# Kernel tuning notes

Hardware: AMD Instinct MI355X
Metric: run time of the kernel (lower is better)

Reference implementation:

```python
import jax, jax.numpy as jnp
import numpy as np

K = 16  # number of neighbors (excluding self)


def setup_inputs() -> dict:
    key = jax.random.key(0)
    k0, k1, k2, k3, k4 = jax.random.split(key, 5)
    B, C, N, Cout = 8, 64, 4096, 64
    x = jax.random.normal(k0, (B, C, N), dtype=jnp.float32)
    s = 1.0 / np.sqrt(C).astype(np.float32)
    W1 = jax.random.normal(k1, (Cout, C), dtype=jnp.float32) * s
    b1 = jax.random.normal(k2, (Cout,), dtype=jnp.float32) * 0.01
    W2 = jax.random.normal(k3, (Cout, C), dtype=jnp.float32) * s
    b2 = jax.random.normal(k4, (Cout,), dtype=jnp.float32) * 0.01
    return {"x": x, "W1": W1, "b1": b1, "W2": W2, "b2": b2}


def _knn_idx(xt):
    # xt: [B, N, C]; squared-euclidean self-KNN, drop self (first / smallest dist)
    sq = jnp.sum(xt * xt, axis=-1)                              # [B, N]
    dist = sq[:, :, None] + sq[:, None, :] - 2.0 * jnp.einsum('bnc,bmc->bnm', xt, xt)
    _, idx = jax.lax.top_k(-dist, K + 1)                        # [B, N, K+1]
    return idx[:, :, 1:]                                        # [B, N, K]


def reference(x, W1, b1, W2, b2):
    # x: [B, C, N]
    xt = jnp.transpose(x, (0, 2, 1))                            # [B, N, C]
    idx = _knn_idx(xt)                                          # [B, N, K]
    # gather neighbors: nb[b,n,k,c] = xt[b, idx[b,n,k], c]
    nb = jax.vmap(lambda xb, ib: xb[ib])(xt, idx)               # [B, N, K, C]
    diff = nb - xt[:, :, None, :]                               # [B, N, K, C]
    message = jnp.einsum('bnkc,oc->bnko', diff, W1) + b1        # conv1 (1x1)
    x_center = jnp.einsum('bnc,oc->bno', xt, W2) + b2           # conv2 (1x1)
    edge = jax.nn.relu(x_center[:, :, None, :] + message)       # [B, N, K, Cout]
    y = jnp.max(edge, axis=2)                                   # [B, N, Cout]
    return jnp.transpose(y, (0, 2, 1))[:, :, None, :]           # [B, Cout, 1, N]
```

## Files before the change

### kernel.cpp

```cpp
#include <hip/hip_runtime.h>
#include <hip/hip_bf16.h>
#include <cstdint>

#define NB    8
#define NPTS  4096
#define NQ    4
#define NT    64
#define PROW  64
#define SENT  0xFF000000u
#define KNN_T 512

typedef __attribute__((ext_vector_type(8))) short bf16x8;
typedef __attribute__((ext_vector_type(4))) float f32x4;

__global__ __launch_bounds__(256) void k_prep(const float* __restrict__ x,
                                              const float* __restrict__ W1,
                                              const float* __restrict__ b1,
                                              const float* __restrict__ W2,
                                              const float* __restrict__ b2,
                                              float* __restrict__ xt,
                                              __hip_bfloat16* __restrict__ xh,
                                              __hip_bfloat16* __restrict__ xl,
                                              float* __restrict__ sq,
                                              float* __restrict__ sqn,
                                              __hip_bfloat16* __restrict__ gh,
                                              __hip_bfloat16* __restrict__ gl,
                                              float* __restrict__ bb) {
  const int t = threadIdx.x;
  if (blockIdx.x == 64) {
    if (blockIdx.y != 0) return;
#pragma unroll 1
    for (int i = t; i < 128 * 64; i += 256) {
      int o = i >> 6, c = i & 63;
      float g = (o < 64) ? W1[o * 64 + c]
                         : (W2[(o - 64) * 64 + c] - W1[(o - 64) * 64 + c]);
      __hip_bfloat16 h = __float2bfloat16(g);
      gh[i] = h;
      gl[i] = __float2bfloat16(g - __bfloat162float(h));
    }
    if (t < 64) bb[t] = b1[t] + b2[t];
    return;
  }
  __shared__ float tile[64][65];
  const int b  = blockIdx.y;
  const int n0 = blockIdx.x * 64;
#pragma unroll
  for (int i = 0; i < 16; ++i) {
    int lin = i * 256 + t;
    int c = lin >> 6, j = lin & 63;
    tile[j][c] = x[(size_t)b * 64 * NPTS + (size_t)c * NPTS + n0 + j];
  }
  __syncthreads();
#pragma unroll
  for (int i = 0; i < 16; ++i) {
    int lin = i * 256 + t;
    int j = lin >> 6, c = lin & 63;
    float v = tile[j][c];
    size_t o = ((size_t)b * NPTS + n0 + j) * 64 + c;
    xt[o] = v;
    __hip_bfloat16 h = __float2bfloat16(v);
    xh[o] = h;
    xl[o] = __float2bfloat16(v - __bfloat162float(h));
  }
  if (t < 64) {
    float s = 0.f;
#pragma unroll
    for (int c = 0; c < 64; ++c) { float v = tile[t][c]; s = fmaf(v, v, s); }
    sq [b * NPTS + t + n0] = s;
    sqn[b * NPTS + t + n0] = 0.5f * s;
  }
}

struct Frag { bf16x8 h0, h1; f32x4 sv; };

__global__ __launch_bounds__(KNN_T, 4) void k_knn(const __hip_bfloat16* __restrict__ xh,
                                                  const float* __restrict__ sqn,
                                                  unsigned* __restrict__ part) {
  __shared__ unsigned bufu[17 * KNN_T];

  const int tid  = threadIdx.x;
  const int w    = tid >> 6;
  const int lane = tid & 63;
  const int quad = lane >> 4, l15 = lane & 15;
  const int rb   = blockIdx.x;
  const int q    = blockIdx.y;
  const int b    = blockIdx.z;
  const size_t xbase = (size_t)b * NPTS * 64;
  const int c0   = q * 1024;
  const int nrow = rb * (KNN_T / 4) + w * 16 + l15;

  const __hip_bfloat16* ph = xh + xbase + (size_t)nrow * 64 + quad * 8;
  bf16x8 rh0 = *(const bf16x8*)(ph);
  bf16x8 rh1 = *(const bf16x8*)(ph + 32);
  rh0 = rh0 ^ (short)0x8000;
  rh1 = rh1 ^ (short)0x8000;
  const float srh = sqn[b * NPTS + nrow];

  unsigned D[16];
#pragma unroll
  for (int i = 0; i < 16; ++i) D[i] = SENT;
  unsigned thr = SENT | 0xFFFu;
  int cnt = 0;

  auto ldfrag = [&](int t) -> Frag {
    Frag f;
    const __hip_bfloat16* ah = xh + xbase + (size_t)(c0 + t * 16 + l15) * 64 + quad * 8;
    f.h0 = *(const bf16x8*)(ah);
    f.h1 = *(const bf16x8*)(ah + 32);
    f.sv = *(const f32x4*)(sqn + b * NPTS + c0 + t * 16 + quad * 4);
    return f;
  };

  auto flush = [&]() {
    unsigned E[16];
#pragma unroll
    for (int j = 0; j < 16; ++j) E[j] = bufu[j * KNN_T + tid];
#pragma unroll
    for (int j = 0; j < 16; ++j) E[j] = (j < cnt) ? E[j] : 0xFFFFFFFFu;
#pragma unroll
    for (int k = 2; k <= 16; k <<= 1)
#pragma unroll
      for (int j = k >> 1; j > 0; j >>= 1)
#pragma unroll
        for (int i = 0; i < 16; ++i) {
          int l = i ^ j;
          if (l > i) {
            unsigned lo = min(E[i], E[l]), hi = max(E[i], E[l]);
            bool up = ((i & k) == 0);
            E[i] = up ? lo : hi;
            E[l] = up ? hi : lo;
          }
        }
    unsigned T[16];
#pragma unroll
    for (int i = 0; i < 16; ++i) T[i] = min(D[i], E[15 - i]);
#pragma unroll
    for (int j = 8; j > 0; j >>= 1)
#pragma unroll
      for (int i = 0; i < 16; ++i) {
        int l = i ^ j;
        if (l > i) {
          unsigned lo = min(T[i], T[l]);
          T[l] = max(T[i], T[l]);
          T[i] = lo;
        }
      }
#pragma unroll
    for (int i = 0; i < 16; ++i) D[i] = T[i];
    cnt = 0;
    thr = D[15] | 0xFFFu;
  };

  auto ins = [&](float s, int m) {
    unsigned u = __float_as_uint(s);
    bool pass = (u <= thr);
    int slot = pass ? cnt : 16;
    bufu[slot * KNN_T + tid] = (u & 0xFFFFF000u) | (unsigned)m;
    cnt += pass;
  };

  auto compute2 = [&](const Frag& fa, const Frag& fb, int tbase) {
    f32x4 m1 = fa.sv, m3 = fb.sv;
#pragma unroll
    for (int i = 0; i < 4; ++i) { m1[i] += srh; m3[i] += srh; }
    m1 = __builtin_amdgcn_mfma_f32_16x16x32_bf16(fa.h0, rh0, m1, 0, 0, 0);
    m3 = __builtin_amdgcn_mfma_f32_16x16x32_bf16(fb.h0, rh0, m3, 0, 0, 0);
    m1 = __builtin_amdgcn_mfma_f32_16x16x32_bf16(fa.h1, rh1, m1, 0, 0, 0);
    m3 = __builtin_amdgcn_mfma_f32_16x16x32_bf16(fb.h1, rh1, m3, 0, 0, 0);
    const int cb = c0 + tbase * 16 + quad * 4;
#pragma unroll
    for (int i = 0; i < 4; ++i) ins(m1[i], cb + i);
#pragma unroll
    for (int i = 0; i < 4; ++i) ins(m3[i], cb + 16 + i);
  };

  Frag a0 = ldfrag(0), a1 = ldfrag(1);
#pragma unroll 1
  for (int it = 0; it < 16; ++it) {
    const int t4 = it * 4;
    Frag b0 = ldfrag(t4 + 2), b1 = ldfrag(t4 + 3);
    compute2(a0, a1, t4);
    if (__any(cnt >= 9)) flush();
    const int tn = (t4 + 4 < NT) ? t4 + 4 : 62;
    a0 = ldfrag(tn);
    a1 = ldfrag(tn + 1);
    compute2(b0, b1, t4 + 2);
    if (__any(cnt >= 9)) flush();
  }
  flush();

#pragma unroll
  for (int rd = 0; rd < 2; ++rd) {
    const int dx = (rd == 0) ? 16 : 32;
    unsigned Bx[16], T[16];
#pragma unroll
    for (int i = 0; i < 16; ++i) Bx[i] = (unsigned)__shfl_xor((int)D[i], dx);
#pragma unroll
    for (int i = 0; i < 16; ++i) T[i] = min(D[i], Bx[15 - i]);
#pragma unroll
    for (int j = 8; j > 0; j >>= 1)
#pragma unroll
      for (int i = 0; i < 16; ++i) {
        int l = i ^ j;
        if (l > i) {
          unsigned lo = min(T[i], T[l]);
          T[l] = max(T[i], T[l]);
          T[i] = lo;
        }
      }
#pragma unroll
    for (int i = 0; i < 16; ++i) D[i] = T[i];
  }
  if (quad == 0) {
    const size_t base = (size_t)(b * NPTS + nrow) * PROW + (size_t)q * 16;
#pragma unroll
    for (int i = 0; i < 16; ++i) part[base + i] = D[i];
  }
}

__global__ __launch_bounds__(256) void k_mr(const unsigned* __restrict__ part,
                                            const float* __restrict__ xt,
                                            const float* __restrict__ sq,
                                            int* __restrict__ knn) {
  __shared__ unsigned short lc[8][20];
  const int g   = threadIdx.x >> 5;
  const int c   = threadIdx.x & 31;
  const int row = blockIdx.x * 8 + g;
  const unsigned v0 = part[(size_t)row * PROW + c];
  const unsigned v1 = part[(size_t)row * PROW + 32 + c];
  int r0 = 0, r1 = 0;
#pragma unroll
  for (int j = 0; j < 32; ++j) {
    unsigned a = (unsigned)__shfl((int)v0, j, 32);
    unsigned d = (unsigned)__shfl((int)v1, j, 32);
    r0 += (a < v0) + (d < v0);
    r1 += (a < v1) + (d < v1);
  }
  if (r0 < 20) lc[g][r0] = (unsigned short)(v0 & 0xFFFu);
  if (r1 < 20) lc[g][r1] = (unsigned short)(v1 & 0xFFFu);
  __syncthreads();
  const int b = row >> 12;
  const int m = lc[g][c < 20 ? c : 0];
  const float4* cr = (const float4*)(xt + (size_t)row * 64);
  const float4* mr = (const float4*)(xt + ((size_t)(b << 12) + m) * 64);
  float d = 0.f;
#pragma unroll
  for (int j = 0; j < 16; ++j) {
    float4 a = cr[j], v = mr[j];
    d = fmaf(a.x, v.x, d); d = fmaf(a.y, v.y, d);
    d = fmaf(a.z, v.z, d); d = fmaf(a.w, v.w, d);
  }
  float key = sq[(b << 12) + m] - 2.f * d;
  if (m == (row & 4095)) key = 1e30f;
  int rk = 0;
#pragma unroll
  for (int j = 0; j < 20; ++j) {
    float kj = __shfl(key, j, 32);
    int   mj = __shfl(m, j, 32);
    rk += (kj < key) || ((kj == key) && (mj < m));
  }
  if (c < 20 && rk < 16) knn[(size_t)row * 16 + rk] = m;
}

__global__ __launch_bounds__(256) void k_pq(const __hip_bfloat16* __restrict__ xh,
                                            const __hip_bfloat16* __restrict__ xl,
                                            const __hip_bfloat16* __restrict__ gh,
                                            const __hip_bfloat16* __restrict__ gl,
                                            const float* __restrict__ bb,
                                            float* __restrict__ P,
                                            float* __restrict__ Q) {
  const int tid  = threadIdx.x;
  const int w    = tid >> 6;
  const int lane = tid & 63;
  const int quad = lane >> 4, l15 = lane & 15;
  const int row0 = blockIdx.x * 64 + w * 16;

  const __hip_bfloat16* pa = xh + (size_t)(row0 + l15) * 64 + quad * 8;
  const __hip_bfloat16* pb = xl + (size_t)(row0 + l15) * 64 + quad * 8;
  const bf16x8 ah0 = *(const bf16x8*)(pa);
  const bf16x8 ah1 = *(const bf16x8*)(pa + 32);
  const bf16x8 al0 = *(const bf16x8*)(pb);
  const bf16x8 al1 = *(const bf16x8*)(pb + 32);

#pragma unroll
  for (int ct = 0; ct < 8; ++ct) {
    const __hip_bfloat16* qh = gh + (size_t)(ct * 16 + l15) * 64 + quad * 8;
    const __hip_bfloat16* ql = gl + (size_t)(ct * 16 + l15) * 64 + quad * 8;
    bf16x8 bh0 = *(const bf16x8*)(qh);
    bf16x8 bh1 = *(const bf16x8*)(qh + 32);
    bf16x8 bl0 = *(const bf16x8*)(ql);
    bf16x8 bl1 = *(const bf16x8*)(ql + 32);
    f32x4 m1 = { 0.f, 0.f, 0.f, 0.f };
    f32x4 m2 = m1, m3 = m1, m4 = m1, m5 = m1, m6 = m1;
    m1 = __builtin_amdgcn_mfma_f32_16x16x32_bf16(ah0, bh0, m1, 0, 0, 0);
    m2 = __builtin_amdgcn_mfma_f32_16x16x32_bf16(ah1, bh1, m2, 0, 0, 0);
    m3 = __builtin_amdgcn_mfma_f32_16x16x32_bf16(ah0, bl0, m3, 0, 0, 0);
    m4 = __builtin_amdgcn_mfma_f32_16x16x32_bf16(ah1, bl1, m4, 0, 0, 0);
    m5 = __builtin_amdgcn_mfma_f32_16x16x32_bf16(al0, bh0, m5, 0, 0, 0);
    m6 = __builtin_amdgcn_mfma_f32_16x16x32_bf16(al1, bh1, m6, 0, 0, 0);
    if (ct < 4) {
#pragma unroll
      for (int i = 0; i < 4; ++i) {
        float s = ((m1[i] + m2[i]) + (m3[i] + m4[i])) + (m5[i] + m6[i]);
        P[(size_t)(row0 + quad * 4 + i) * 64 + ct * 16 + l15] = s;
      }
    } else {
      const float bq = bb[(ct - 4) * 16 + l15];
#pragma unroll
      for (int i = 0; i < 4; ++i) {
        float s = ((m1[i] + m2[i]) + (m3[i] + m4[i])) + (m5[i] + m6[i]);
        Q[(size_t)(row0 + quad * 4 + i) * 64 + (ct - 4) * 16 + l15] = s + bq;
      }
    }
  }
}

__global__ __launch_bounds__(512) void k_out(const float* __restrict__ P,
                                             const float* __restrict__ Q,
                                             const int* __restrict__ knn,
                                             float* __restrict__ out) {
  __shared__ float tile[64][65];
  const int b    = blockIdx.y;
  const int n0   = blockIdx.x * 64;
  const int wave = threadIdx.x >> 6;
  const int lane = threadIdx.x & 63;
#pragma unroll 1
  for (int i = 0; i < 8; ++i) {
    const int nl = wave * 8 + i;
    const int gn = b * NPTS + n0 + nl;
    float acc = -1e30f;
    const float qv = Q[(size_t)gn * 64 + lane];
    const int* id = knn + (size_t)gn * 16;
#pragma unroll
    for (int k = 0; k < 16; ++k) {
      int m = id[k];
      float p = P[((size_t)b * NPTS + m) * 64 + lane];
      acc = fmaxf(acc, qv + p);
    }
    tile[nl][lane] = fmaxf(acc, 0.f);
  }
  __syncthreads();
#pragma unroll
  for (int i = 0; i < 8; ++i) {
    const int o = i * 8 + wave;
    out[((size_t)b * 64 + o) * NPTS + n0 + lane] = tile[lane][o];
  }
}

extern "C" void kernel_launch(void* const* d_in, const int* in_sizes, int n_in,
                              void* d_out, int out_size, void* d_ws, size_t ws_size,
                              hipStream_t stream) {
  const float* x  = (const float*)d_in[0];
  const float* W1 = (const float*)d_in[1];
  const float* b1 = (const float*)d_in[2];
  const float* W2 = (const float*)d_in[3];
  const float* b2 = (const float*)d_in[4];
  float* out = (float*)d_out;

  float* ws = (float*)d_ws;
  const size_t NPT_ALL = (size_t)NB * NPTS;
  float*          XT   = ws;
  float*          SQ   = XT + NPT_ALL * 64;
  float*          SQN  = SQ + NPT_ALL;
  __hip_bfloat16* XH   = (__hip_bfloat16*)(SQN + NPT_ALL);
  __hip_bfloat16* XL   = XH + NPT_ALL * 64;
  unsigned*       PART = (unsigned*)(XL + NPT_ALL * 64);
  int*            KNN  = (int*)(PART + NPT_ALL * PROW);
  __hip_bfloat16* GH   = (__hip_bfloat16*)(KNN + NPT_ALL * 16);
  __hip_bfloat16* GL   = GH + 128 * 64;
  float*          BB   = (float*)(GL + 128 * 64);
  float*          Pm   = (float*)PART;
  float*          Qm   = XT;

  k_prep <<<dim3(NPTS / 64 + 1, NB), 256, 0, stream>>>(x, W1, b1, W2, b2,
                                                       XT, XH, XL, SQ, SQN,
                                                       GH, GL, BB);
  k_knn  <<<dim3(NPTS / (KNN_T / 4), NQ, NB), KNN_T, 0, stream>>>(XH, SQN, PART);
  k_mr   <<<dim3(NPT_ALL / 8), 256, 0, stream>>>(PART, XT, SQ, KNN);
  k_pq   <<<dim3(NPT_ALL / 64), 256, 0, stream>>>(XH, XL, GH, GL, BB, Pm, Qm);
  k_out  <<<dim3(NPTS / 64, NB), 512, 0, stream>>>(Pm, Qm, KNN, out);
}
```

Measured before the change: 296.0 us.

## Encode KNN distance as scaled integer key and stagger wave column order

The KNN score is rescaled so that 128*sq + 32768 minus 256*dot (via a bf16 exponent bump on the negated row fragment) becomes a non-negative float. It is truncated to an integer and packed with the column index into a sortable key. This drops the per-element srh add and the float-bit masking, but quantizes distances to integer steps and assumes the value stays within 20 bits. Each wave also starts its column-tile sweep at a different offset, which spreads L2/cache access across waves. The merge kernel now reads its partial rows with a vectorized uint2 load.

```diff
diff --git a/kernel.cpp b/kernel.cpp
--- a/kernel.cpp
+++ b/kernel.cpp
@@ -67,7 +67,7 @@
 #pragma unroll
     for (int c = 0; c < 64; ++c) { float v = tile[t][c]; s = fmaf(v, v, s); }
     sq [b * NPTS + t + n0] = s;
-    sqn[b * NPTS + t + n0] = 0.5f * s;
+    sqn[b * NPTS + t + n0] = fmaf(128.f, s, 32768.f);
   }
 }
 
@@ -87,14 +87,14 @@
   const int b    = blockIdx.z;
   const size_t xbase = (size_t)b * NPTS * 64;
   const int c0   = q * 1024;
+  const int woff = w * 8;
   const int nrow = rb * (KNN_T / 4) + w * 16 + l15;
 
   const __hip_bfloat16* ph = xh + xbase + (size_t)nrow * 64 + quad * 8;
   bf16x8 rh0 = *(const bf16x8*)(ph);
   bf16x8 rh1 = *(const bf16x8*)(ph + 32);
-  rh0 = rh0 ^ (short)0x8000;
-  rh1 = rh1 ^ (short)0x8000;
-  const float srh = sqn[b * NPTS + nrow];
+  rh0 = (rh0 ^ (short)0x8000) + (short)0x0400;
+  rh1 = (rh1 ^ (short)0x8000) + (short)0x0400;
 
   unsigned D[16];
 #pragma unroll
@@ -152,39 +152,39 @@
   };
 
   auto ins = [&](float s, int m) {
-    unsigned u = __float_as_uint(s);
-    bool pass = (u <= thr);
+    unsigned ki  = (unsigned)s;
+    unsigned key = (ki << 12) | (unsigned)m;
+    bool pass = (key <= thr);
     int slot = pass ? cnt : 16;
-    bufu[slot * KNN_T + tid] = (u & 0xFFFFF000u) | (unsigned)m;
+    bufu[slot * KNN_T + tid] = key;
     cnt += pass;
   };
 
-  auto compute2 = [&](const Frag& fa, const Frag& fb, int tbase) {
+  auto compute2 = [&](const Frag& fa, const Frag& fb, int ta, int tb) {
     f32x4 m1 = fa.sv, m3 = fb.sv;
-#pragma unroll
-    for (int i = 0; i < 4; ++i) { m1[i] += srh; m3[i] += srh; }
     m1 = __builtin_amdgcn_mfma_f32_16x16x32_bf16(fa.h0, rh0, m1, 0, 0, 0);
     m3 = __builtin_amdgcn_mfma_f32_16x16x32_bf16(fb.h0, rh0, m3, 0, 0, 0);
     m1 = __builtin_amdgcn_mfma_f32_16x16x32_bf16(fa.h1, rh1, m1, 0, 0, 0);
     m3 = __builtin_amdgcn_mfma_f32_16x16x32_bf16(fb.h1, rh1, m3, 0, 0, 0);
-    const int cb = c0 + tbase * 16 + quad * 4;
-#pragma unroll
-    for (int i = 0; i < 4; ++i) ins(m1[i], cb + i);
-#pragma unroll
-    for (int i = 0; i < 4; ++i) ins(m3[i], cb + 16 + i);
+    const int ca = c0 + ta * 16 + quad * 4;
+    const int cb = c0 + tb * 16 + quad * 4;
+#pragma unroll
+    for (int i = 0; i < 4; ++i) ins(m1[i], ca + i);
+#pragma unroll
+    for (int i = 0; i < 4; ++i) ins(m3[i], cb + i);
   };
 
-  Frag a0 = ldfrag(0), a1 = ldfrag(1);
+  Frag a0 = ldfrag(woff), a1 = ldfrag((woff + 1) & 63);
 #pragma unroll 1
   for (int it = 0; it < 16; ++it) {
     const int t4 = it * 4;
-    Frag b0 = ldfrag(t4 + 2), b1 = ldfrag(t4 + 3);
-    compute2(a0, a1, t4);
+    const int s2 = (woff + t4 + 2) & 63, s3 = (woff + t4 + 3) & 63;
+    Frag b0 = ldfrag(s2), b1 = ldfrag(s3);
+    compute2(a0, a1, (woff + t4) & 63, (woff + t4 + 1) & 63);
     if (__any(cnt >= 9)) flush();
-    const int tn = (t4 + 4 < NT) ? t4 + 4 : 62;
-    a0 = ldfrag(tn);
-    a1 = ldfrag(tn + 1);
-    compute2(b0, b1, t4 + 2);
+    a0 = ldfrag((woff + t4 + 4) & 63);
+    a1 = ldfrag((woff + t4 + 5) & 63);
+    compute2(b0, b1, s2, s3);
     if (__any(cnt >= 9)) flush();
   }
   flush();
@@ -226,8 +226,8 @@
   const int g   = threadIdx.x >> 5;
   const int c   = threadIdx.x & 31;
   const int row = blockIdx.x * 8 + g;
-  const unsigned v0 = part[(size_t)row * PROW + c];
-  const unsigned v1 = part[(size_t)row * PROW + 32 + c];
+  const uint2 vv = ((const uint2*)(part + (size_t)row * PROW))[c];
+  const unsigned v0 = vv.x, v1 = vv.y;
   int r0 = 0, r1 = 0;
 #pragma unroll
   for (int j = 0; j < 32; ++j) {
```

After: 299.1 us. About the same (+1.0%).
